# Optimization experiments

Hardware: AMD Instinct MI355X
Metric: run time of the kernel (lower is better)

## Reference

```python
import jax, jax.numpy as jnp
import numpy as np

N = 50000      # nodes
E = 800000     # edges
F_IN = 128     # numInputFeatures
HID = 64       # numHiddenLayerFeatures
C = 40         # numClasses


def setup_inputs() -> dict:
    key = jax.random.key(0)
    ks = jax.random.split(key, 24)
    def nrm(k, shape, s=0.05):
        return jax.random.normal(k, shape, jnp.float32) * s
    return {
        "x": jax.random.normal(ks[0], (N, F_IN), jnp.float32),
        "edge_index": jax.random.randint(ks[1], (2, E), 0, N, jnp.int64),
        "w": jax.random.normal(ks[2], (3,), jnp.float32),  # ensemble weights
        # GCNConv
        "W_gcn": nrm(ks[3], (F_IN, HID)), "b_gcn": jnp.zeros((HID,), jnp.float32),
        # SAGEConv (lin_l on aggregated neighbors w/ bias, lin_r on root no bias)
        "Wl_sage": nrm(ks[4], (F_IN, HID)), "bl_sage": jnp.zeros((HID,), jnp.float32),
        "Wr_sage": nrm(ks[5], (F_IN, HID)),
        # GATConv heads=1
        "W_gat": nrm(ks[6], (F_IN, HID)), "att_src": nrm(ks[7], (HID,)),
        "att_dst": nrm(ks[8], (HID,)), "b_gat": jnp.zeros((HID,), jnp.float32),
        # TransformerConv heads=1 (hidden -> classes)
        "Wq": nrm(ks[9], (HID, C)), "bq": jnp.zeros((C,), jnp.float32),
        "Wk": nrm(ks[10], (HID, C)), "bk": jnp.zeros((C,), jnp.float32),
        "Wv": nrm(ks[11], (HID, C)), "bv": jnp.zeros((C,), jnp.float32),
        "Wskip": nrm(ks[12], (HID, C)), "bskip": jnp.zeros((C,), jnp.float32),
    }


def _segment_softmax(e, seg, num_segments):
    m = jax.ops.segment_max(e, seg, num_segments=num_segments)
    ex = jnp.exp(e - m[seg])
    s = jax.ops.segment_sum(ex, seg, num_segments=num_segments)
    return ex / (s[seg] + 1e-16)


def _gcn(x, src, dst, W, b):
    h = x @ W                                        # [N, HID]
    loop = jnp.arange(N, dtype=src.dtype)
    s = jnp.concatenate([src, loop]); d = jnp.concatenate([dst, loop])
    deg = jax.ops.segment_sum(jnp.ones_like(d, jnp.float32), d, num_segments=N)
    dinv = jnp.where(deg > 0, jax.lax.rsqrt(deg), 0.0)
    norm = dinv[s] * dinv[d]                         # [E+N]
    out = jax.ops.segment_sum(h[s] * norm[:, None], d, num_segments=N)
    return out + b


def _sage(x, src, dst, Wl, bl, Wr):
    cnt = jax.ops.segment_sum(jnp.ones((src.shape[0],), jnp.float32), dst, num_segments=N)
    agg = jax.ops.segment_sum(x[src], dst, num_segments=N) / jnp.maximum(cnt, 1.0)[:, None]
    return agg @ Wl + bl + x @ Wr


def _gat(x, src, dst, W, att_src, att_dst, b):
    h = x @ W                                        # [N, HID]
    loop = jnp.arange(N, dtype=src.dtype)
    s = jnp.concatenate([src, loop]); d = jnp.concatenate([dst, loop])
    a_s = h @ att_src; a_d = h @ att_dst             # [N]
    e = jax.nn.leaky_relu(a_s[s] + a_d[d], 0.2)
    alpha = _segment_softmax(e, d, N)
    out = jax.ops.segment_sum(alpha[:, None] * h[s], d, num_segments=N)
    return out + b


def _transformer(x, src, dst, Wq, bq, Wk, bk, Wv, bv, Wskip, bskip):
    q = x @ Wq + bq; k = x @ Wk + bk; v = x @ Wv + bv  # [N, C]
    score = jnp.sum(q[dst] * k[src], axis=-1) / jnp.sqrt(jnp.float32(C))
    alpha = _segment_softmax(score, dst, N)
    out = jax.ops.segment_sum(alpha[:, None] * v[src], dst, num_segments=N)
    return out + (x @ Wskip + bskip)


def reference(x, edge_index, w, W_gcn, b_gcn, Wl_sage, bl_sage, Wr_sage,
              W_gat, att_src, att_dst, b_gat,
              Wq, bq, Wk, bk, Wv, bv, Wskip, bskip):
    src, dst = edge_index[0], edge_index[1]
    gelu = lambda t: jax.nn.gelu(t, approximate=False)
    ens = gelu(_gcn(x, src, dst, W_gcn, b_gcn)) * w[0]
    ens = ens + gelu(_sage(x, src, dst, Wl_sage, bl_sage, Wr_sage)) * w[1]
    ens = ens + gelu(_gat(x, src, dst, W_gat, att_src, att_dst, b_gat)) * w[2]
    out = _transformer(ens, src, dst, Wq, bq, Wk, bk, Wv, bv, Wskip, bskip)
    return jax.nn.log_softmax(out, axis=1)
```

## Files before the change

### kernel.cpp

```cpp
#include <hip/hip_runtime.h>
#include <math.h>

#define NN 50000
#define EE 800000
#define FIN 128
#define HID 64
#define CL 40
#define SCB 256
#define NBLK ((NN + SCB - 1) / SCB)
#define NREP 8
#define QW 256
#define HGW 192

typedef unsigned short ushort_t;
typedef unsigned int uint_t;
typedef float f32x4 __attribute__((ext_vector_type(4)));
typedef short s16x8 __attribute__((ext_vector_type(8)));

__device__ __forceinline__ ushort_t f2bf(float f) {
  uint_t u = __float_as_uint(f);
  u = (u + 0x7FFFu + ((u >> 16) & 1u)) >> 16;
  return (ushort_t)u;
}
__device__ __forceinline__ uint_t f2bf2(float lo, float hi) {
  return (uint_t)f2bf(lo) | ((uint_t)f2bf(hi) << 16);
}
__device__ __forceinline__ float bf2f(ushort_t s) {
  return __uint_as_float(((uint_t)s) << 16);
}
__device__ __forceinline__ float bflo(uint_t u) {
  return __uint_as_float(u << 16);
}
__device__ __forceinline__ float bfhi(uint_t u) {
  return __uint_as_float(u & 0xFFFF0000u);
}

__device__ __forceinline__ int wave_sum_i(int v) {
#pragma unroll
  for (int off = 32; off > 0; off >>= 1) v += __shfl_xor(v, off, 64);
  return v;
}
__device__ __forceinline__ float half_sum(float v) {
#pragma unroll
  for (int off = 16; off > 0; off >>= 1) v += __shfl_xor(v, off, 64);
  return v;
}
__device__ __forceinline__ float half_max(float v) {
#pragma unroll
  for (int off = 16; off > 0; off >>= 1) v = fmaxf(v, __shfl_xor(v, off, 64));
  return v;
}
__device__ __forceinline__ float gelu_exact(float x) {
  return 0.5f * x * (1.0f + erff(x * 0.70710678118654752f));
}
__device__ __forceinline__ float leaky02(float x) {
  return x >= 0.f ? x : 0.2f * x;
}

#define PREP_W 169
#define PREP_HIST 3125
__global__ __launch_bounds__(256) void k_prep(
    const int* __restrict__ dst,
    const float* __restrict__ W0, const float* __restrict__ W1,
    const float* __restrict__ W2, const float* __restrict__ W3,
    const float* __restrict__ Q0, const float* __restrict__ Q1,
    const float* __restrict__ Q2, const float* __restrict__ Q3,
    const float* __restrict__ b0, const float* __restrict__ b1,
    const float* __restrict__ b2, const float* __restrict__ b3,
    ushort_t* __restrict__ WtA, ushort_t* __restrict__ WtB,
    float* __restrict__ bcat, int* __restrict__ cntR,
    int* __restrict__ erank) {
  int b = blockIdx.x, t = threadIdx.x;
  if (b < PREP_W) {
    int idx = b * 256 + t;
    if (idx < 32768) {
      int m = idx >> 13, r = idx & 8191, c = r >> 7, k = r & 127;
      const float* W = (m == 0) ? W0 : (m == 1) ? W1 : (m == 2) ? W2 : W3;
      WtA[idx] = f2bf(W[k * HID + c]);
    } else if (idx < 43008) {
      int j = idx - 32768;
      int c = j >> 6, k = j & 63;
      int mm = c / CL, cc = c % CL;
      const float* W = (mm == 0) ? Q0 : (mm == 1) ? Q1 : (mm == 2) ? Q2 : Q3;
      WtB[j] = f2bf(W[k * CL + cc]);
    } else if (idx < 43168) {
      int c = idx - 43008;
      int mm = c / CL, cc = c % CL;
      const float* bb = (mm == 0) ? b0 : (mm == 1) ? b1 : (mm == 2) ? b2 : b3;
      bcat[c] = bb[cc];
    }
  } else {
    int hb = b - PREP_W;
    int e = hb * 256 + t;
    if (e < EE) {
      int r = hb & (NREP - 1);
      erank[e] = atomicAdd(&cntR[(size_t)r * NN + dst[e]], 1);
    }
  }
}

__global__ __launch_bounds__(256) void k_gemmA(
    const float* __restrict__ x, const ushort_t* __restrict__ WtA,
    const float* __restrict__ attS, const float* __restrict__ attD,
    ushort_t* __restrict__ Hg, ushort_t* __restrict__ hroot,
    float* __restrict__ a_s, float* __restrict__ a_d) {
  __shared__ __align__(16) ushort_t wlds[64 * 136];
  const int t = threadIdx.x;
  const int wv = t >> 6, l = t & 63;
  const int lr = l & 15, lg = l >> 4;
  const int rbase = blockIdx.x * 64 + wv * 16;
  int arow = rbase + lr;
  int arowc = arow < NN ? arow : NN - 1;
  const float* xp = x + (size_t)arowc * 128 + lg * 8;
  s16x8 af[4];
#pragma unroll
  for (int ks = 0; ks < 4; ++ks) {
    float4 v0 = *(const float4*)(xp + ks * 32);
    float4 v1 = *(const float4*)(xp + ks * 32 + 4);
    s16x8 a;
    a[0] = (short)f2bf(v0.x); a[1] = (short)f2bf(v0.y);
    a[2] = (short)f2bf(v0.z); a[3] = (short)f2bf(v0.w);
    a[4] = (short)f2bf(v1.x); a[5] = (short)f2bf(v1.y);
    a[6] = (short)f2bf(v1.z); a[7] = (short)f2bf(v1.w);
    af[ks] = a;
  }
  for (int m = 0; m < 4; ++m) {
    if (m) __syncthreads();
    for (int idx = t; idx < 64 * 16; idx += 256) {
      int c = idx >> 4, ch = idx & 15;
      *(uint4*)&wlds[c * 136 + ch * 8] =
          *(const uint4*)(WtA + m * 8192 + c * 128 + ch * 8);
    }
    __syncthreads();
    f32x4 acc[4] = {};
#pragma unroll
    for (int ks = 0; ks < 4; ++ks) {
#pragma unroll
      for (int n = 0; n < 4; ++n) {
        s16x8 bf = *(const s16x8*)&wlds[(n * 16 + lr) * 136 + ks * 32 + lg * 8];
        acc[n] =
            __builtin_amdgcn_mfma_f32_16x16x32_bf16(af[ks], bf, acc[n], 0, 0, 0);
      }
    }
#pragma unroll
    for (int n = 0; n < 4; ++n) {
#pragma unroll
      for (int j = 0; j < 4; ++j) {
        int orow = rbase + lg * 4 + j;
        if (orow < NN) {
          if (m < 3)
            Hg[(size_t)orow * HGW + m * 64 + n * 16 + lr] = f2bf(acc[n][j]);
          else
            hroot[(size_t)orow * 64 + n * 16 + lr] = f2bf(acc[n][j]);
        }
      }
    }
    if (m == 2) {
      float sat[4], dat[4];
#pragma unroll
      for (int n = 0; n < 4; ++n) {
        sat[n] = attS[n * 16 + lr];
        dat[n] = attD[n * 16 + lr];
      }
#pragma unroll
      for (int j = 0; j < 4; ++j) {
        float ps = 0.f, pd = 0.f;
#pragma unroll
        for (int n = 0; n < 4; ++n) {
          ps = fmaf(acc[n][j], sat[n], ps);
          pd = fmaf(acc[n][j], dat[n], pd);
        }
#pragma unroll
        for (int off = 1; off < 16; off <<= 1) {
          ps += __shfl_xor(ps, off, 64);
          pd += __shfl_xor(pd, off, 64);
        }
        int orow = rbase + lg * 4 + j;
        if (lr == 0 && orow < NN) { a_s[orow] = ps; a_d[orow] = pd; }
      }
    }
  }
}

__global__ __launch_bounds__(SCB) void k_bsum(const int* __restrict__ cntR,
                                              int* __restrict__ bsum) {
  __shared__ int wsm[4];
  int i = blockIdx.x * SCB + threadIdx.x;
  int v = 0;
  if (i < NN) {
#pragma unroll
    for (int r = 0; r < NREP; ++r) v += cntR[(size_t)r * NN + i];
  }
  int s = wave_sum_i(v);
  int lane = threadIdx.x & 63, wv = threadIdx.x >> 6;
  if (lane == 0) wsm[wv] = s;
  __syncthreads();
  if (threadIdx.x == 0) bsum[blockIdx.x] = wsm[0] + wsm[1] + wsm[2] + wsm[3];
}

__global__ __launch_bounds__(SCB) void k_scanapply(
    const int* __restrict__ cntR, const int* __restrict__ bsum,
    const float* __restrict__ a_s, const float* __restrict__ a_d,
    int* __restrict__ cnt, int* __restrict__ offs, int* __restrict__ base8,
    float* __restrict__ dinv, float2* __restrict__ auxS,
    float2* __restrict__ auxD) {
  __shared__ int ts[SCB];
  __shared__ int wred[4];
  int b = blockIdx.x, t = threadIdx.x;
  int pv = (t < b) ? bsum[t] : 0;
  int ps = wave_sum_i(pv);
  int lane = t & 63, wv = t >> 6;
  if (lane == 0) wred[wv] = ps;
  int i = b * SCB + t;
  int cr[NREP];
  int v = 0;
  if (i < NN) {
#pragma unroll
    for (int r = 0; r < NREP; ++r) {
      cr[r] = cntR[(size_t)r * NN + i];
      v += cr[r];
    }
  }
  ts[t] = v;
  __syncthreads();
  int prefix = wred[0] + wred[1] + wred[2] + wred[3];
  for (int off = 1; off < SCB; off <<= 1) {
    int u = (t >= off) ? ts[t - off] : 0;
    __syncthreads();
    ts[t] += u;
    __syncthreads();
  }
  if (i < NN) {
    int ex = ts[t] - v + prefix;
    offs[i] = ex;
    cnt[i] = v;
    float dv = rsqrtf((float)v + 1.0f);
    dinv[i] = dv;
    auxS[i] = make_float2(dv, a_s[i]);
    auxD[i] = make_float2(dv, a_d[i]);
    int run = ex;
#pragma unroll
    for (int r = 0; r < NREP; ++r) {
      base8[(size_t)i * NREP + r] = run;
      run += cr[r];
    }
  }
}

__global__ __launch_bounds__(256) void k_sc1(const int* __restrict__ dst,
                                             const int* __restrict__ erank,
                                             const int* __restrict__ base8,
                                             int* __restrict__ esorted) {
  int e = blockIdx.x * blockDim.x + threadIdx.x;
  if (e < EE) {
    int d = dst[e];
    int r = (e >> 8) & (NREP - 1);
    esorted[base8[(size_t)d * NREP + r] + erank[e]] = e;
  }
}

__global__ __launch_bounds__(256) void k_sc2(
    const int* __restrict__ esorted, const int* __restrict__ src,
    const int* __restrict__ dst, const float2* __restrict__ auxS,
    const float2* __restrict__ auxD, int* __restrict__ srcidx,
    int* __restrict__ dsts, float2* __restrict__ edata) {
  int p = blockIdx.x * blockDim.x + threadIdx.x;
  if (p < EE) {
    int e = esorted[p];
    int s = src[e], d = dst[e];
    srcidx[p] = s;
    dsts[p] = d;
    float2 A = auxS[s];
    float2 B = auxD[d];
    float ex = __expf(leaky02(A.y + B.y));
    edata[p] = make_float2(A.x * B.x, ex);
  }
}

__global__ __launch_bounds__(256) void k_agg1(
    const int* __restrict__ srcidx, const int* __restrict__ offs,
    const int* __restrict__ cnt, const ushort_t* __restrict__ Hg,
    const ushort_t* __restrict__ hroot, const float2* __restrict__ edata,
    const float* __restrict__ dinv, const float* __restrict__ a_s,
    const float* __restrict__ a_d, const float* __restrict__ b_gcn,
    const float* __restrict__ bl, const float* __restrict__ b_gat,
    const float* __restrict__ w, ushort_t* __restrict__ ensb) {
  int node = (blockIdx.x * blockDim.x + threadIdx.x) >> 6;
  int lane = threadIdx.x & 63;
  if (node >= NN) return;
  const int half = lane >> 5;
  const int fl = lane & 31;
  int beg = offs[node];
  int c = cnt[node];
  int end = beg + c;
  float ag0 = 0.f, ag1 = 0.f, as0 = 0.f, as1 = 0.f, aa0 = 0.f, aa1 = 0.f,
        dg = 0.f;
  int p = beg + half;
  for (; p + 6 < end; p += 8) {
    int sA = srcidx[p], sB = srcidx[p + 2], sC = srcidx[p + 4],
        sD = srcidx[p + 6];
    float2 eA = edata[p], eB = edata[p + 2], eC = edata[p + 4],
           eD = edata[p + 6];
    const uint_t* hA = (const uint_t*)(Hg + (size_t)sA * HGW);
    const uint_t* hB = (const uint_t*)(Hg + (size_t)sB * HGW);
    const uint_t* hC = (const uint_t*)(Hg + (size_t)sC * HGW);
    const uint_t* hD = (const uint_t*)(Hg + (size_t)sD * HGW);
    uint_t gA = hA[fl], qA = hA[32 + fl], tA = hA[64 + fl];
    uint_t gB = hB[fl], qB = hB[32 + fl], tB = hB[64 + fl];
    uint_t gC = hC[fl], qC = hC[32 + fl], tC = hC[64 + fl];
    uint_t gD = hD[fl], qD = hD[32 + fl], tD = hD[64 + fl];
    ag0 = fmaf(bflo(gA), eA.x, ag0); ag1 = fmaf(bfhi(gA), eA.x, ag1);
    ag0 = fmaf(bflo(gB), eB.x, ag0); ag1 = fmaf(bfhi(gB), eB.x, ag1);
    ag0 = fmaf(bflo(gC), eC.x, ag0); ag1 = fmaf(bfhi(gC), eC.x, ag1);
    ag0 = fmaf(bflo(gD), eD.x, ag0); ag1 = fmaf(bfhi(gD), eD.x, ag1);
    as0 += (bflo(qA) + bflo(qB)) + (bflo(qC) + bflo(qD));
    as1 += (bfhi(qA) + bfhi(qB)) + (bfhi(qC) + bfhi(qD));
    aa0 = fmaf(bflo(tA), eA.y, aa0); aa1 = fmaf(bfhi(tA), eA.y, aa1);
    aa0 = fmaf(bflo(tB), eB.y, aa0); aa1 = fmaf(bfhi(tB), eB.y, aa1);
    aa0 = fmaf(bflo(tC), eC.y, aa0); aa1 = fmaf(bfhi(tC), eC.y, aa1);
    aa0 = fmaf(bflo(tD), eD.y, aa0); aa1 = fmaf(bfhi(tD), eD.y, aa1);
    dg += (eA.y + eB.y) + (eC.y + eD.y);
  }
  for (; p < end; p += 2) {
    int sA = srcidx[p];
    float2 eA = edata[p];
    const uint_t* hA = (const uint_t*)(Hg + (size_t)sA * HGW);
    uint_t gA = hA[fl], qA = hA[32 + fl], tA = hA[64 + fl];
    ag0 = fmaf(bflo(gA), eA.x, ag0); ag1 = fmaf(bfhi(gA), eA.x, ag1);
    as0 += bflo(qA);                 as1 += bfhi(qA);
    aa0 = fmaf(bflo(tA), eA.y, aa0); aa1 = fmaf(bfhi(tA), eA.y, aa1);
    dg += eA.y;
  }
  ag0 += __shfl_xor(ag0, 32, 64); ag1 += __shfl_xor(ag1, 32, 64);
  as0 += __shfl_xor(as0, 32, 64); as1 += __shfl_xor(as1, 32, 64);
  aa0 += __shfl_xor(aa0, 32, 64); aa1 += __shfl_xor(aa1, 32, 64);
  dg += __shfl_xor(dg, 32, 64);
  float dd = dinv[node];
  float exl = __expf(leaky02(a_s[node] + a_d[node]));
  const uint_t* hd = (const uint_t*)(Hg + (size_t)node * HGW);
  uint_t hg = hd[fl], ht = hd[64 + fl];
  uint_t hr = ((const uint_t*)hroot)[(size_t)node * 32 + fl];
  float2 bg = ((const float2*)b_gcn)[fl];
  float2 bs = ((const float2*)bl)[fl];
  float2 ba = ((const float2*)b_gat)[fl];
  float dd2 = dd * dd;
  float cinv = 1.0f / fmaxf((float)c, 1.0f);
  float gdi = 1.0f / (dg + exl + 1e-16f);
  float g0 = ag0 + dd2 * bflo(hg) + bg.x;
  float g1 = ag1 + dd2 * bfhi(hg) + bg.y;
  float s0 = as0 * cinv + bs.x + bflo(hr);
  float s1 = as1 * cinv + bs.y + bfhi(hr);
  float t0 = (aa0 + exl * bflo(ht)) * gdi + ba.x;
  float t1 = (aa1 + exl * bfhi(ht)) * gdi + ba.y;
  float w0 = w[0], w1 = w[1], w2 = w[2];
  float e0 = w0 * gelu_exact(g0) + w1 * gelu_exact(s0) + w2 * gelu_exact(t0);
  float e1 = w0 * gelu_exact(g1) + w1 * gelu_exact(s1) + w2 * gelu_exact(t1);
  if (half == 0) ((uint_t*)ensb)[(size_t)node * 32 + fl] = f2bf2(e0, e1);
}

__global__ __launch_bounds__(256) void k_gemmB(
    const ushort_t* __restrict__ ensb, const ushort_t* __restrict__ WtB,
    const float* __restrict__ bcat, ushort_t* __restrict__ QKVSb) {
  __shared__ __align__(16) ushort_t wb[160 * 72];
  __shared__ float bsh[160];
  const int t = threadIdx.x;
  for (int idx = t; idx < 160 * 8; idx += 256) {
    int c = idx >> 3, ch = idx & 7;
    *(uint4*)&wb[c * 72 + ch * 8] = *(const uint4*)(WtB + c * 64 + ch * 8);
  }
  if (t < 160) bsh[t] = bcat[t];
  __syncthreads();
  const int wv = t >> 6, l = t & 63;
  const int lr = l & 15, lg = l >> 4;
  const int rbase = blockIdx.x * 64 + wv * 16;
  int arow = rbase + lr;
  int arowc = arow < NN ? arow : NN - 1;
  const ushort_t* ap = ensb + (size_t)arowc * 64 + lg * 8;
  f32x4 acc[10] = {};
#pragma unroll
  for (int ks = 0; ks < 2; ++ks) {
    s16x8 af = *(const s16x8*)(ap + ks * 32);
#pragma unroll
    for (int n = 0; n < 10; ++n) {
      s16x8 bf = *(const s16x8*)&wb[(n * 16 + lr) * 72 + ks * 32 + lg * 8];
      acc[n] = __builtin_amdgcn_mfma_f32_16x16x32_bf16(af, bf, acc[n], 0, 0, 0);
    }
  }
#pragma unroll
  for (int n = 0; n < 10; ++n) {
    int col = n * 16 + lr;
    int seg = col / CL;
    int off = seg * 64 + (col - seg * CL);
#pragma unroll
    for (int j = 0; j < 4; ++j) {
      int orow = rbase + lg * 4 + j;
      if (orow < NN)
        QKVSb[(size_t)orow * QW + off] = f2bf(acc[n][j] + bsh[col]);
    }
  }
}

__global__ __launch_bounds__(256) void k_score(
    const int* __restrict__ srcidx, const int* __restrict__ dsts,
    const ushort_t* __restrict__ QKVSb, float* __restrict__ escore) {
  int p = (blockIdx.x * 256 + threadIdx.x) >> 3;
  int l = threadIdx.x & 7;
  if (p >= EE) return;
  int s = srcidx[p], d = dsts[p];
  float part = 0.f;
  if (l < 5) {
    const uint4 qv = *(const uint4*)(QKVSb + (size_t)d * QW + l * 8);
    const uint4 kv = *(const uint4*)(QKVSb + (size_t)s * QW + 64 + l * 8);
    part = bflo(qv.x) * bflo(kv.x);
    part = fmaf(bfhi(qv.x), bfhi(kv.x), part);
    part = fmaf(bflo(qv.y), bflo(kv.y), part);
    part = fmaf(bfhi(qv.y), bfhi(kv.y), part);
    part = fmaf(bflo(qv.z), bflo(kv.z), part);
    part = fmaf(bfhi(qv.z), bfhi(kv.z), part);
    part = fmaf(bflo(qv.w), bflo(kv.w), part);
    part = fmaf(bfhi(qv.w), bfhi(kv.w), part);
  }
  part += __shfl_xor(part, 1, 64);
  part += __shfl_xor(part, 2, 64);
  part += __shfl_xor(part, 4, 64);
  if (l == 0) escore[p] = __expf(part * 0.15811388300841897f);
}

__global__ __launch_bounds__(256) void k_agg2(
    const int* __restrict__ srcidx, const int* __restrict__ offs,
    const int* __restrict__ cnt, const ushort_t* __restrict__ QKVSb,
    const float* __restrict__ escore, float* __restrict__ out) {
  int node = (blockIdx.x * blockDim.x + threadIdx.x) >> 6;
  int lane = threadIdx.x & 63;
  if (node >= NN) return;
  const int half = lane >> 5;
  const int fl = lane & 31;
  const bool valid = fl < 20;
  int beg = offs[node];
  int end = beg + cnt[node];
  float den = 0.f, av0 = 0.f, av1 = 0.f;
  const int VOFF = 64;
  int p = beg + half;
  for (; p + 6 < end; p += 8) {
    int sA = srcidx[p], sB = srcidx[p + 2], sC = srcidx[p + 4],
        sD = srcidx[p + 6];
    float eA = escore[p], eB = escore[p + 2], eC = escore[p + 4],
          eD = escore[p + 6];
    uint_t vA = valid ? ((const uint_t*)QKVSb)[(size_t)sA * 128 + VOFF + fl] : 0u;
    uint_t vB = valid ? ((const uint_t*)QKVSb)[(size_t)sB * 128 + VOFF + fl] : 0u;
    uint_t vC = valid ? ((const uint_t*)QKVSb)[(size_t)sC * 128 + VOFF + fl] : 0u;
    uint_t vD = valid ? ((const uint_t*)QKVSb)[(size_t)sD * 128 + VOFF + fl] : 0u;
    av0 = fmaf(eA, bflo(vA), av0); av1 = fmaf(eA, bfhi(vA), av1);
    av0 = fmaf(eB, bflo(vB), av0); av1 = fmaf(eB, bfhi(vB), av1);
    av0 = fmaf(eC, bflo(vC), av0); av1 = fmaf(eC, bfhi(vC), av1);
    av0 = fmaf(eD, bflo(vD), av0); av1 = fmaf(eD, bfhi(vD), av1);
    den += (eA + eB) + (eC + eD);
  }
  for (; p < end; p += 2) {
    int sA = srcidx[p];
    float eA = escore[p];
    uint_t vA = valid ? ((const uint_t*)QKVSb)[(size_t)sA * 128 + VOFF + fl] : 0u;
    av0 = fmaf(eA, bflo(vA), av0); av1 = fmaf(eA, bfhi(vA), av1);
    den += eA;
  }
  av0 += __shfl_xor(av0, 32, 64);
  av1 += __shfl_xor(av1, 32, 64);
  den += __shfl_xor(den, 32, 64);
  uint_t sk = valid ? ((const uint_t*)QKVSb)[(size_t)node * 128 + 96 + fl] : 0u;
  float di = 1.0f / (den + 1e-16f);
  float o0 = valid ? av0 * di + bflo(sk) : -3.0e38f;
  float o1 = valid ? av1 * di + bfhi(sk) : -3.0e38f;
  float m = half_max(fmaxf(o0, o1));
  float eo = valid ? __expf(o0 - m) + __expf(o1 - m) : 0.f;
  float ls = logf(half_sum(eo));
  if (valid && half == 0) {
    float2 r = make_float2(o0 - m - ls, o1 - m - ls);
    ((float2*)out)[(size_t)node * 20 + fl] = r;
  }
}

extern "C" void kernel_launch(void* const* d_in, const int* in_sizes, int n_in,
                              void* d_out, int out_size, void* d_ws,
                              size_t ws_size, hipStream_t stream) {
  const float* x     = (const float*)d_in[0];
  const int*   ei    = (const int*)d_in[1];
  const float* w     = (const float*)d_in[2];
  const float* W_gcn = (const float*)d_in[3];
  const float* b_gcn = (const float*)d_in[4];
  const float* Wl    = (const float*)d_in[5];
  const float* bl    = (const float*)d_in[6];
  const float* Wr    = (const float*)d_in[7];
  const float* W_gat = (const float*)d_in[8];
  const float* att_s = (const float*)d_in[9];
  const float* att_d = (const float*)d_in[10];
  const float* b_gat = (const float*)d_in[11];
  const float* Wq    = (const float*)d_in[12];
  const float* bq    = (const float*)d_in[13];
  const float* Wk    = (const float*)d_in[14];
  const float* bk    = (const float*)d_in[15];
  const float* Wv    = (const float*)d_in[16];
  const float* bv    = (const float*)d_in[17];
  const float* Wsk   = (const float*)d_in[18];
  const float* bsk   = (const float*)d_in[19];
  float* out = (float*)d_out;
  float* ws  = (float*)d_ws;

  const int* src = ei;
  const int* dst = ei + EE;

  ushort_t* Hg     = (ushort_t*)ws;
  ushort_t* hroot  = (ushort_t*)(ws + (size_t)96 * NN);
  ushort_t* ensb   = (ushort_t*)(ws + (size_t)128 * NN);
  float*    a_s    = ws + (size_t)160 * NN;
  float*    a_d    = ws + (size_t)161 * NN;
  float*    dinv   = ws + (size_t)162 * NN;
  ushort_t* qkvsb  = (ushort_t*)(ws + (size_t)163 * NN);
  ushort_t* WtA    = (ushort_t*)(ws + (size_t)291 * NN);
  ushort_t* WtB    = (ushort_t*)(ws + (size_t)291 * NN + 16384);
  float*    bcat   = ws + (size_t)291 * NN + 21504;
  float*    escore = ws + (size_t)291 * NN + 21664;
  float2*   edata  = (float2*)(ws + (size_t)291 * NN + 21664 + EE);
  float2*   auxS   = (float2*)(ws + (size_t)291 * NN + 21664 + 3 * (size_t)EE);
  float2*   auxD   = auxS + NN;
  int*      ibase  = (int*)(ws + (size_t)295 * NN + 21664 + 3 * (size_t)EE);
  int*      cnt    = ibase;
  int*      offs   = ibase + NN;
  int*      srcidx = ibase + 2 * NN;
  int*      dsts   = ibase + 2 * NN + EE;
  int*      erank  = ibase + 2 * NN + 2 * EE;
  int*      esorted= ibase + 2 * NN + 3 * EE;
  int*      bsum   = ibase + 2 * NN + 4 * EE;
  int*      cntR   = ibase + 2 * NN + 4 * EE + 256;
  int*      base8  = cntR + (size_t)NREP * NN;

  hipMemsetAsync(cntR, 0, (size_t)NREP * NN * sizeof(int), stream);

  k_prep<<<PREP_W + PREP_HIST, 256, 0, stream>>>(
      dst, W_gcn, Wl, W_gat, Wr, Wq, Wk, Wv, Wsk, bq, bk, bv, bsk, WtA, WtB,
      bcat, cntR, erank);

  k_gemmA<<<(NN + 63) / 64, 256, 0, stream>>>(x, WtA, att_s, att_d, Hg, hroot,
                                              a_s, a_d);
  k_bsum<<<NBLK, SCB, 0, stream>>>(cntR, bsum);
  k_scanapply<<<NBLK, SCB, 0, stream>>>(cntR, bsum, a_s, a_d, cnt, offs, base8,
                                        dinv, auxS, auxD);
  k_sc1<<<(EE + 255) / 256, 256, 0, stream>>>(dst, erank, base8, esorted);
  k_sc2<<<(EE + 255) / 256, 256, 0, stream>>>(esorted, src, dst, auxS, auxD,
                                              srcidx, dsts, edata);
  k_agg1<<<(NN + 3) / 4, 256, 0, stream>>>(srcidx, offs, cnt, Hg, hroot, edata,
                                           dinv, a_s, a_d, b_gcn, bl, b_gat, w,
                                           ensb);
  k_gemmB<<<(NN + 63) / 64, 256, 0, stream>>>(ensb, WtB, bcat, qkvsb);
  k_score<<<(EE * 8 + 255) / 256, 256, 0, stream>>>(srcidx, dsts, qkvsb,
                                                    escore);
  k_agg2<<<(NN + 3) / 4, 256, 0, stream>>>(srcidx, offs, cnt, qkvsb, escore,
                                           out);
}
```

Before: 219.3 us.

## Aggregate raw bf16 inputs before projecting, and fold attention vectors into weights

```diff
diff --git a/kernel.cpp b/kernel.cpp
--- a/kernel.cpp
+++ b/kernel.cpp
@@ -10,7 +10,6 @@
 #define NBLK ((NN + SCB - 1) / SCB)
 #define NREP 8
 #define QW 256
-#define HGW 192
 
 typedef unsigned short ushort_t;
 typedef unsigned int uint_t;
@@ -25,9 +24,6 @@
 __device__ __forceinline__ uint_t f2bf2(float lo, float hi) {
   return (uint_t)f2bf(lo) | ((uint_t)f2bf(hi) << 16);
 }
-__device__ __forceinline__ float bf2f(ushort_t s) {
-  return __uint_as_float(((uint_t)s) << 16);
-}
 __device__ __forceinline__ float bflo(uint_t u) {
   return __uint_as_float(u << 16);
 }
@@ -36,6 +32,11 @@
 }
 
 __device__ __forceinline__ int wave_sum_i(int v) {
+#pragma unroll
+  for (int off = 32; off > 0; off >>= 1) v += __shfl_xor(v, off, 64);
+  return v;
+}
+__device__ __forceinline__ float wave_sum_f(float v) {
 #pragma unroll
   for (int off = 32; off > 0; off >>= 1) v += __shfl_xor(v, off, 64);
   return v;
@@ -67,9 +68,10 @@
     const float* __restrict__ Q2, const float* __restrict__ Q3,
     const float* __restrict__ b0, const float* __restrict__ b1,
     const float* __restrict__ b2, const float* __restrict__ b3,
+    const float* __restrict__ attS, const float* __restrict__ attD,
     ushort_t* __restrict__ WtA, ushort_t* __restrict__ WtB,
-    float* __restrict__ bcat, int* __restrict__ cntR,
-    int* __restrict__ erank) {
+    float* __restrict__ bcat, float* __restrict__ wv,
+    int* __restrict__ cntR, int* __restrict__ erank) {
   int b = blockIdx.x, t = threadIdx.x;
   if (b < PREP_W) {
     int idx = b * 256 + t;
@@ -89,97 +91,38 @@
       const float* bb = (mm == 0) ? b0 : (mm == 1) ? b1 : (mm == 2) ? b2 : b3;
       bcat[c] = bb[cc];
     }
-  } else {
+  } else if (b < PREP_W + PREP_HIST) {
     int hb = b - PREP_W;
     int e = hb * 256 + t;
     if (e < EE) {
       int r = hb & (NREP - 1);
       erank[e] = atomicAdd(&cntR[(size_t)r * NN + dst[e]], 1);
     }
-  }
-}
-
-__global__ __launch_bounds__(256) void k_gemmA(
-    const float* __restrict__ x, const ushort_t* __restrict__ WtA,
-    const float* __restrict__ attS, const float* __restrict__ attD,
-    ushort_t* __restrict__ Hg, ushort_t* __restrict__ hroot,
-    float* __restrict__ a_s, float* __restrict__ a_d) {
-  __shared__ __align__(16) ushort_t wlds[64 * 136];
-  const int t = threadIdx.x;
-  const int wv = t >> 6, l = t & 63;
-  const int lr = l & 15, lg = l >> 4;
-  const int rbase = blockIdx.x * 64 + wv * 16;
-  int arow = rbase + lr;
-  int arowc = arow < NN ? arow : NN - 1;
-  const float* xp = x + (size_t)arowc * 128 + lg * 8;
-  s16x8 af[4];
-#pragma unroll
-  for (int ks = 0; ks < 4; ++ks) {
-    float4 v0 = *(const float4*)(xp + ks * 32);
-    float4 v1 = *(const float4*)(xp + ks * 32 + 4);
-    s16x8 a;
-    a[0] = (short)f2bf(v0.x); a[1] = (short)f2bf(v0.y);
-    a[2] = (short)f2bf(v0.z); a[3] = (short)f2bf(v0.w);
-    a[4] = (short)f2bf(v1.x); a[5] = (short)f2bf(v1.y);
-    a[6] = (short)f2bf(v1.z); a[7] = (short)f2bf(v1.w);
-    af[ks] = a;
-  }
-  for (int m = 0; m < 4; ++m) {
-    if (m) __syncthreads();
-    for (int idx = t; idx < 64 * 16; idx += 256) {
-      int c = idx >> 4, ch = idx & 15;
-      *(uint4*)&wlds[c * 136 + ch * 8] =
-          *(const uint4*)(WtA + m * 8192 + c * 128 + ch * 8);
-    }
-    __syncthreads();
-    f32x4 acc[4] = {};
-#pragma unroll
-    for (int ks = 0; ks < 4; ++ks) {
-#pragma unroll
-      for (int n = 0; n < 4; ++n) {
-        s16x8 bf = *(const s16x8*)&wlds[(n * 16 + lr) * 136 + ks * 32 + lg * 8];
-        acc[n] =
-            __builtin_amdgcn_mfma_f32_16x16x32_bf16(af[ks], bf, acc[n], 0, 0, 0);
-      }
-    }
-#pragma unroll
-    for (int n = 0; n < 4; ++n) {
-#pragma unroll
-      for (int j = 0; j < 4; ++j) {
-        int orow = rbase + lg * 4 + j;
-        if (orow < NN) {
-          if (m < 3)
-            Hg[(size_t)orow * HGW + m * 64 + n * 16 + lr] = f2bf(acc[n][j]);
-          else
-            hroot[(size_t)orow * 64 + n * 16 + lr] = f2bf(acc[n][j]);
-        }
-      }
-    }
-    if (m == 2) {
-      float sat[4], dat[4];
-#pragma unroll
-      for (int n = 0; n < 4; ++n) {
-        sat[n] = attS[n * 16 + lr];
-        dat[n] = attD[n * 16 + lr];
-      }
-#pragma unroll
-      for (int j = 0; j < 4; ++j) {
-        float ps = 0.f, pd = 0.f;
-#pragma unroll
-        for (int n = 0; n < 4; ++n) {
-          ps = fmaf(acc[n][j], sat[n], ps);
-          pd = fmaf(acc[n][j], dat[n], pd);
-        }
-#pragma unroll
-        for (int off = 1; off < 16; off <<= 1) {
-          ps += __shfl_xor(ps, off, 64);
-          pd += __shfl_xor(pd, off, 64);
-        }
-        int orow = rbase + lg * 4 + j;
-        if (lr == 0 && orow < NN) { a_s[orow] = ps; a_d[orow] = pd; }
-      }
-    }
-  }
+  } else {
+    int which = t >> 7, k = t & 127;
+    const float* att = which ? attD : attS;
+    float s = 0.f;
+    for (int c = 0; c < HID; ++c) s = fmaf(W2[k * HID + c], att[c], s);
+    wv[which * FIN + k] = s;
+  }
+}
+
+__global__ __launch_bounds__(256) void k_xcast(
+    const float* __restrict__ x, const float* __restrict__ wv,
+    uint_t* __restrict__ xbu, float* __restrict__ a_s,
+    float* __restrict__ a_d) {
+  int node = (blockIdx.x * blockDim.x + threadIdx.x) >> 6;
+  int l = threadIdx.x & 63;
+  if (node >= NN) return;
+  float2 xv = ((const float2*)x)[(size_t)node * 64 + l];
+  float2 wsv = ((const float2*)wv)[l];
+  float2 wdv = ((const float2*)(wv + FIN))[l];
+  float ps = fmaf(xv.x, wsv.x, xv.y * wsv.y);
+  float pd = fmaf(xv.x, wdv.x, xv.y * wdv.y);
+  ps = wave_sum_f(ps);
+  pd = wave_sum_f(pd);
+  xbu[(size_t)node * 64 + l] = f2bf2(xv.x, xv.y);
+  if (l == 0) { a_s[node] = ps; a_d[node] = pd; }
 }
 
 __global__ __launch_bounds__(SCB) void k_bsum(const int* __restrict__ cntR,
@@ -277,14 +220,12 @@
   }
 }
 
-__global__ __launch_bounds__(256) void k_agg1(
+__global__ __launch_bounds__(256) void k_agg1x(
     const int* __restrict__ srcidx, const int* __restrict__ offs,
-    const int* __restrict__ cnt, const ushort_t* __restrict__ Hg,
-    const ushort_t* __restrict__ hroot, const float2* __restrict__ edata,
-    const float* __restrict__ dinv, const float* __restrict__ a_s,
-    const float* __restrict__ a_d, const float* __restrict__ b_gcn,
-    const float* __restrict__ bl, const float* __restrict__ b_gat,
-    const float* __restrict__ w, ushort_t* __restrict__ ensb) {
+    const int* __restrict__ cnt, const uint_t* __restrict__ xbu,
+    const float2* __restrict__ edata, const float* __restrict__ dinv,
+    const float* __restrict__ a_s, const float* __restrict__ a_d,
+    uint_t* __restrict__ aggu) {
   int node = (blockIdx.x * blockDim.x + threadIdx.x) >> 6;
   int lane = threadIdx.x & 63;
   if (node >= NN) return;
@@ -293,69 +234,141 @@
   int beg = offs[node];
   int c = cnt[node];
   int end = beg + c;
-  float ag0 = 0.f, ag1 = 0.f, as0 = 0.f, as1 = 0.f, aa0 = 0.f, aa1 = 0.f,
-        dg = 0.f;
+  float g0 = 0.f, g1 = 0.f, g2 = 0.f, g3 = 0.f;
+  float s0 = 0.f, s1 = 0.f, s2 = 0.f, s3 = 0.f;
+  float t0 = 0.f, t1 = 0.f, t2 = 0.f, t3 = 0.f;
+  float dg = 0.f;
   int p = beg + half;
   for (; p + 6 < end; p += 8) {
     int sA = srcidx[p], sB = srcidx[p + 2], sC = srcidx[p + 4],
         sD = srcidx[p + 6];
     float2 eA = edata[p], eB = edata[p + 2], eC = edata[p + 4],
            eD = edata[p + 6];
-    const uint_t* hA = (const uint_t*)(Hg + (size_t)sA * HGW);
-    const uint_t* hB = (const uint_t*)(Hg + (size_t)sB * HGW);
-    const uint_t* hC = (const uint_t*)(Hg + (size_t)sC * HGW);
-    const uint_t* hD = (const uint_t*)(Hg + (size_t)sD * HGW);
-    uint_t gA = hA[fl], qA = hA[32 + fl], tA = hA[64 + fl];
-    uint_t gB = hB[fl], qB = hB[32 + fl], tB = hB[64 + fl];
-    uint_t gC = hC[fl], qC = hC[32 + fl], tC = hC[64 + fl];
-    uint_t gD = hD[fl], qD = hD[32 + fl], tD = hD[64 + fl];
-    ag0 = fmaf(bflo(gA), eA.x, ag0); ag1 = fmaf(bfhi(gA), eA.x, ag1);
-    ag0 = fmaf(bflo(gB), eB.x, ag0); ag1 = fmaf(bfhi(gB), eB.x, ag1);
-    ag0 = fmaf(bflo(gC), eC.x, ag0); ag1 = fmaf(bfhi(gC), eC.x, ag1);
-    ag0 = fmaf(bflo(gD), eD.x, ag0); ag1 = fmaf(bfhi(gD), eD.x, ag1);
-    as0 += (bflo(qA) + bflo(qB)) + (bflo(qC) + bflo(qD));
-    as1 += (bfhi(qA) + bfhi(qB)) + (bfhi(qC) + bfhi(qD));
-    aa0 = fmaf(bflo(tA), eA.y, aa0); aa1 = fmaf(bfhi(tA), eA.y, aa1);
-    aa0 = fmaf(bflo(tB), eB.y, aa0); aa1 = fmaf(bfhi(tB), eB.y, aa1);
-    aa0 = fmaf(bflo(tC), eC.y, aa0); aa1 = fmaf(bfhi(tC), eC.y, aa1);
-    aa0 = fmaf(bflo(tD), eD.y, aa0); aa1 = fmaf(bfhi(tD), eD.y, aa1);
+    const uint_t* xA = xbu + (size_t)sA * 64;
+    const uint_t* xB = xbu + (size_t)sB * 64;
+    const uint_t* xC = xbu + (size_t)sC * 64;
+    const uint_t* xD = xbu + (size_t)sD * 64;
+    uint_t a0 = xA[fl], a1 = xA[32 + fl];
+    uint_t b0 = xB[fl], b1 = xB[32 + fl];
+    uint_t c0 = xC[fl], c1 = xC[32 + fl];
+    uint_t d0 = xD[fl], d1 = xD[32 + fl];
+    float A0 = bflo(a0), A1 = bfhi(a0), A2 = bflo(a1), A3 = bfhi(a1);
+    float B0 = bflo(b0), B1 = bfhi(b0), B2 = bflo(b1), B3 = bfhi(b1);
+    float C0 = bflo(c0), C1 = bfhi(c0), C2 = bflo(c1), C3 = bfhi(c1);
+    float D0 = bflo(d0), D1 = bfhi(d0), D2 = bflo(d1), D3 = bfhi(d1);
+    g0 = fmaf(A0, eA.x, g0); g1 = fmaf(A1, eA.x, g1);
+    g2 = fmaf(A2, eA.x, g2); g3 = fmaf(A3, eA.x, g3);
+    g0 = fmaf(B0, eB.x, g0); g1 = fmaf(B1, eB.x, g1);
+    g2 = fmaf(B2, eB.x, g2); g3 = fmaf(B3, eB.x, g3);
+    g0 = fmaf(C0, eC.x, g0); g1 = fmaf(C1, eC.x, g1);
+    g2 = fmaf(C2, eC.x, g2); g3 = fmaf(C3, eC.x, g3);
+    g0 = fmaf(D0, eD.x, g0); g1 = fmaf(D1, eD.x, g1);
+    g2 = fmaf(D2, eD.x, g2); g3 = fmaf(D3, eD.x, g3);
+    s0 += (A0 + B0) + (C0 + D0); s1 += (A1 + B1) + (C1 + D1);
+    s2 += (A2 + B2) + (C2 + D2); s3 += (A3 + B3) + (C3 + D3);
+    t0 = fmaf(A0, eA.y, t0); t1 = fmaf(A1, eA.y, t1);
+    t2 = fmaf(A2, eA.y, t2); t3 = fmaf(A3, eA.y, t3);
+    t0 = fmaf(B0, eB.y, t0); t1 = fmaf(B1, eB.y, t1);
+    t2 = fmaf(B2, eB.y, t2); t3 = fmaf(B3, eB.y, t3);
+    t0 = fmaf(C0, eC.y, t0); t1 = fmaf(C1, eC.y, t1);
+    t2 = fmaf(C2, eC.y, t2); t3 = fmaf(C3, eC.y, t3);
+    t0 = fmaf(D0, eD.y, t0); t1 = fmaf(D1, eD.y, t1);
+    t2 = fmaf(D2, eD.y, t2); t3 = fmaf(D3, eD.y, t3);
     dg += (eA.y + eB.y) + (eC.y + eD.y);
   }
   for (; p < end; p += 2) {
     int sA = srcidx[p];
     float2 eA = edata[p];
-    const uint_t* hA = (const uint_t*)(Hg + (size_t)sA * HGW);
-    uint_t gA = hA[fl], qA = hA[32 + fl], tA = hA[64 + fl];
-    ag0 = fmaf(bflo(gA), eA.x, ag0); ag1 = fmaf(bfhi(gA), eA.x, ag1);
-    as0 += bflo(qA);                 as1 += bfhi(qA);
-    aa0 = fmaf(bflo(tA), eA.y, aa0); aa1 = fmaf(bfhi(tA), eA.y, aa1);
+    const uint_t* xA = xbu + (size_t)sA * 64;
+    uint_t a0 = xA[fl], a1 = xA[32 + fl];
+    float A0 = bflo(a0), A1 = bfhi(a0), A2 = bflo(a1), A3 = bfhi(a1);
+    g0 = fmaf(A0, eA.x, g0); g1 = fmaf(A1, eA.x, g1);
+    g2 = fmaf(A2, eA.x, g2); g3 = fmaf(A3, eA.x, g3);
+    s0 += A0; s1 += A1; s2 += A2; s3 += A3;
+    t0 = fmaf(A0, eA.y, t0); t1 = fmaf(A1, eA.y, t1);
+    t2 = fmaf(A2, eA.y, t2); t3 = fmaf(A3, eA.y, t3);
     dg += eA.y;
   }
-  ag0 += __shfl_xor(ag0, 32, 64); ag1 += __shfl_xor(ag1, 32, 64);
-  as0 += __shfl_xor(as0, 32, 64); as1 += __shfl_xor(as1, 32, 64);
-  aa0 += __shfl_xor(aa0, 32, 64); aa1 += __shfl_xor(aa1, 32, 64);
+  g0 += __shfl_xor(g0, 32, 64); g1 += __shfl_xor(g1, 32, 64);
+  g2 += __shfl_xor(g2, 32, 64); g3 += __shfl_xor(g3, 32, 64);
+  s0 += __shfl_xor(s0, 32, 64); s1 += __shfl_xor(s1, 32, 64);
+  s2 += __shfl_xor(s2, 32, 64); s3 += __shfl_xor(s3, 32, 64);
+  t0 += __shfl_xor(t0, 32, 64); t1 += __shfl_xor(t1, 32, 64);
+  t2 += __shfl_xor(t2, 32, 64); t3 += __shfl_xor(t3, 32, 64);
   dg += __shfl_xor(dg, 32, 64);
   float dd = dinv[node];
   float exl = __expf(leaky02(a_s[node] + a_d[node]));
-  const uint_t* hd = (const uint_t*)(Hg + (size_t)node * HGW);
-  uint_t hg = hd[fl], ht = hd[64 + fl];
-  uint_t hr = ((const uint_t*)hroot)[(size_t)node * 32 + fl];
-  float2 bg = ((const float2*)b_gcn)[fl];
-  float2 bs = ((const float2*)bl)[fl];
-  float2 ba = ((const float2*)b_gat)[fl];
+  const uint_t* xn = xbu + (size_t)node * 64;
+  uint_t n0 = xn[fl], n1 = xn[32 + fl];
+  float X0 = bflo(n0), X1 = bfhi(n0), X2 = bflo(n1), X3 = bfhi(n1);
   float dd2 = dd * dd;
+  g0 = fmaf(X0, dd2, g0); g1 = fmaf(X1, dd2, g1);
+  g2 = fmaf(X2, dd2, g2); g3 = fmaf(X3, dd2, g3);
+  t0 = fmaf(X0, exl, t0); t1 = fmaf(X1, exl, t1);
+  t2 = fmaf(X2, exl, t2); t3 = fmaf(X3, exl, t3);
   float cinv = 1.0f / fmaxf((float)c, 1.0f);
   float gdi = 1.0f / (dg + exl + 1e-16f);
-  float g0 = ag0 + dd2 * bflo(hg) + bg.x;
-  float g1 = ag1 + dd2 * bfhi(hg) + bg.y;
-  float s0 = as0 * cinv + bs.x + bflo(hr);
-  float s1 = as1 * cinv + bs.y + bfhi(hr);
-  float t0 = (aa0 + exl * bflo(ht)) * gdi + ba.x;
-  float t1 = (aa1 + exl * bfhi(ht)) * gdi + ba.y;
+  s0 *= cinv; s1 *= cinv; s2 *= cinv; s3 *= cinv;
+  t0 *= gdi; t1 *= gdi; t2 *= gdi; t3 *= gdi;
+  if (half == 0) {
+    uint_t* ag = aggu + (size_t)node * 192;
+    ag[fl] = f2bf2(g0, g1);       ag[32 + fl] = f2bf2(g2, g3);
+    ag[64 + fl] = f2bf2(s0, s1);  ag[96 + fl] = f2bf2(s2, s3);
+    ag[128 + fl] = f2bf2(t0, t1); ag[160 + fl] = f2bf2(t2, t3);
+  }
+}
+
+__global__ __launch_bounds__(256) void k_post(
+    const ushort_t* __restrict__ agg, const ushort_t* __restrict__ xb,
+    const ushort_t* __restrict__ WtA, const float* __restrict__ b_gcn,
+    const float* __restrict__ bl, const float* __restrict__ b_gat,
+    const float* __restrict__ w, ushort_t* __restrict__ ensb) {
+  __shared__ __align__(16) ushort_t wlds[64 * 136];
+  const int t = threadIdx.x;
+  const int wv = t >> 6, l = t & 63;
+  const int lr = l & 15, lg = l >> 4;
+  const int rbase = blockIdx.x * 64 + wv * 16;
+  int arow = rbase + lr;
+  int arowc = arow < NN ? arow : NN - 1;
+  f32x4 acc[4][4] = {};
+#pragma unroll
+  for (int m = 0; m < 4; ++m) {
+    if (m) __syncthreads();
+    for (int idx = t; idx < 64 * 16; idx += 256) {
+      int c = idx >> 4, ch = idx & 15;
+      *(uint4*)&wlds[c * 136 + ch * 8] =
+          *(const uint4*)(WtA + m * 8192 + c * 128 + ch * 8);
+    }
+    __syncthreads();
+    const ushort_t* ap = (m < 3) ? agg + (size_t)arowc * 384 + m * 128 + lg * 8
+                                 : xb + (size_t)arowc * 128 + lg * 8;
+#pragma unroll
+    for (int ks = 0; ks < 4; ++ks) {
+      s16x8 af = *(const s16x8*)(ap + ks * 32);
+#pragma unroll
+      for (int n = 0; n < 4; ++n) {
+        s16x8 bf = *(const s16x8*)&wlds[(n * 16 + lr) * 136 + ks * 32 + lg * 8];
+        acc[m][n] =
+            __builtin_amdgcn_mfma_f32_16x16x32_bf16(af, bf, acc[m][n], 0, 0, 0);
+      }
+    }
+  }
   float w0 = w[0], w1 = w[1], w2 = w[2];
-  float e0 = w0 * gelu_exact(g0) + w1 * gelu_exact(s0) + w2 * gelu_exact(t0);
-  float e1 = w0 * gelu_exact(g1) + w1 * gelu_exact(s1) + w2 * gelu_exact(t1);
-  if (half == 0) ((uint_t*)ensb)[(size_t)node * 32 + fl] = f2bf2(e0, e1);
+#pragma unroll
+  for (int n = 0; n < 4; ++n) {
+    int col = n * 16 + lr;
+    float bgv = b_gcn[col], bsv = bl[col], bav = b_gat[col];
+#pragma unroll
+    for (int j = 0; j < 4; ++j) {
+      int orow = rbase + lg * 4 + j;
+      if (orow < NN) {
+        float g = gelu_exact(acc[0][n][j] + bgv);
+        float s = gelu_exact(acc[1][n][j] + acc[3][n][j] + bsv);
+        float tt = gelu_exact(acc[2][n][j] + bav);
+        ensb[(size_t)orow * 64 + col] = f2bf(w0 * g + w1 * s + w2 * tt);
+      }
+    }
+  }
 }
 
 __global__ __launch_bounds__(256) void k_gemmB(
@@ -403,27 +416,25 @@
 __global__ __launch_bounds__(256) void k_score(
     const int* __restrict__ srcidx, const int* __restrict__ dsts,
     const ushort_t* __restrict__ QKVSb, float* __restrict__ escore) {
-  int p = (blockIdx.x * 256 + threadIdx.x) >> 3;
-  int l = threadIdx.x & 7;
+  int p = blockIdx.x * 256 + threadIdx.x;
   if (p >= EE) return;
   int s = srcidx[p], d = dsts[p];
-  float part = 0.f;
-  if (l < 5) {
-    const uint4 qv = *(const uint4*)(QKVSb + (size_t)d * QW + l * 8);
-    const uint4 kv = *(const uint4*)(QKVSb + (size_t)s * QW + 64 + l * 8);
-    part = bflo(qv.x) * bflo(kv.x);
-    part = fmaf(bfhi(qv.x), bfhi(kv.x), part);
-    part = fmaf(bflo(qv.y), bflo(kv.y), part);
-    part = fmaf(bfhi(qv.y), bfhi(kv.y), part);
-    part = fmaf(bflo(qv.z), bflo(kv.z), part);
-    part = fmaf(bfhi(qv.z), bfhi(kv.z), part);
-    part = fmaf(bflo(qv.w), bflo(kv.w), part);
-    part = fmaf(bfhi(qv.w), bfhi(kv.w), part);
-  }
-  part += __shfl_xor(part, 1, 64);
-  part += __shfl_xor(part, 2, 64);
-  part += __shfl_xor(part, 4, 64);
-  if (l == 0) escore[p] = __expf(part * 0.15811388300841897f);
+  const uint4* qp = (const uint4*)(QKVSb + (size_t)d * QW);
+  const uint4* kp = (const uint4*)(QKVSb + (size_t)s * QW + 64);
+  float dot = 0.f;
+#pragma unroll
+  for (int i = 0; i < 5; ++i) {
+    uint4 q = qp[i], k = kp[i];
+    dot = fmaf(bflo(q.x), bflo(k.x), dot);
+    dot = fmaf(bfhi(q.x), bfhi(k.x), dot);
+    dot = fmaf(bflo(q.y), bflo(k.y), dot);
+    dot = fmaf(bfhi(q.y), bfhi(k.y), dot);
+    dot = fmaf(bflo(q.z), bflo(k.z), dot);
+    dot = fmaf(bfhi(q.z), bfhi(k.z), dot);
+    dot = fmaf(bflo(q.w), bflo(k.w), dot);
+    dot = fmaf(bfhi(q.w), bfhi(k.w), dot);
+  }
+  escore[p] = __expf(dot * 0.15811388300841897f);
 }
 
 __global__ __launch_bounds__(256) void k_agg2(
@@ -508,21 +519,22 @@
   const int* src = ei;
   const int* dst = ei + EE;
 
-  ushort_t* Hg     = (ushort_t*)ws;
-  ushort_t* hroot  = (ushort_t*)(ws + (size_t)96 * NN);
-  ushort_t* ensb   = (ushort_t*)(ws + (size_t)128 * NN);
-  float*    a_s    = ws + (size_t)160 * NN;
-  float*    a_d    = ws + (size_t)161 * NN;
-  float*    dinv   = ws + (size_t)162 * NN;
-  ushort_t* qkvsb  = (ushort_t*)(ws + (size_t)163 * NN);
-  ushort_t* WtA    = (ushort_t*)(ws + (size_t)291 * NN);
-  ushort_t* WtB    = (ushort_t*)(ws + (size_t)291 * NN + 16384);
-  float*    bcat   = ws + (size_t)291 * NN + 21504;
-  float*    escore = ws + (size_t)291 * NN + 21664;
-  float2*   edata  = (float2*)(ws + (size_t)291 * NN + 21664 + EE);
-  float2*   auxS   = (float2*)(ws + (size_t)291 * NN + 21664 + 3 * (size_t)EE);
-  float2*   auxD   = auxS + NN;
-  int*      ibase  = (int*)(ws + (size_t)295 * NN + 21664 + 3 * (size_t)EE);
+  uint_t*   xbu    = (uint_t*)ws;
+  uint_t*   aggu   = (uint_t*)(ws + (size_t)64 * NN);
+  ushort_t* ensb   = (ushort_t*)(ws + (size_t)256 * NN);
+  float*    a_s    = ws + (size_t)288 * NN;
+  float*    a_d    = ws + (size_t)289 * NN;
+  float*    dinv   = ws + (size_t)290 * NN;
+  ushort_t* qkvsb  = (ushort_t*)(ws + (size_t)291 * NN);
+  float2*   auxS   = (float2*)(ws + (size_t)419 * NN);
+  float2*   auxD   = (float2*)(ws + (size_t)421 * NN);
+  float*    wv     = ws + (size_t)423 * NN;
+  ushort_t* WtA    = (ushort_t*)(ws + (size_t)423 * NN + 256);
+  ushort_t* WtB    = (ushort_t*)(ws + (size_t)423 * NN + 16640);
+  float*    bcat   = ws + (size_t)423 * NN + 21760;
+  float*    escore = ws + (size_t)423 * NN + 21920;
+  float2*   edata  = (float2*)(ws + (size_t)423 * NN + 21920 + EE);
+  int*      ibase  = (int*)(ws + (size_t)423 * NN + 21920 + 3 * (size_t)EE);
   int*      cnt    = ibase;
   int*      offs   = ibase + NN;
   int*      srcidx = ibase + 2 * NN;
@@ -535,24 +547,24 @@
 
   hipMemsetAsync(cntR, 0, (size_t)NREP * NN * sizeof(int), stream);
 
-  k_prep<<<PREP_W + PREP_HIST, 256, 0, stream>>>(
-      dst, W_gcn, Wl, W_gat, Wr, Wq, Wk, Wv, Wsk, bq, bk, bv, bsk, WtA, WtB,
-      bcat, cntR, erank);
-
-  k_gemmA<<<(NN + 63) / 64, 256, 0, stream>>>(x, WtA, att_s, att_d, Hg, hroot,
-                                              a_s, a_d);
+  k_prep<<<PREP_W + PREP_HIST + 1, 256, 0, stream>>>(
+      dst, W_gcn, Wl, W_gat, Wr, Wq, Wk, Wv, Wsk, bq, bk, bv, bsk, att_s,
+      att_d, WtA, WtB, bcat, wv, cntR, erank);
+
+  k_xcast<<<(NN + 3) / 4, 256, 0, stream>>>(x, wv, xbu, a_s, a_d);
   k_bsum<<<NBLK, SCB, 0, stream>>>(cntR, bsum);
   k_scanapply<<<NBLK, SCB, 0, stream>>>(cntR, bsum, a_s, a_d, cnt, offs, base8,
                                         dinv, auxS, auxD);
   k_sc1<<<(EE + 255) / 256, 256, 0, stream>>>(dst, erank, base8, esorted);
   k_sc2<<<(EE + 255) / 256, 256, 0, stream>>>(esorted, src, dst, auxS, auxD,
                                               srcidx, dsts, edata);
-  k_agg1<<<(NN + 3) / 4, 256, 0, stream>>>(srcidx, offs, cnt, Hg, hroot, edata,
-                                           dinv, a_s, a_d, b_gcn, bl, b_gat, w,
-                                           ensb);
+  k_agg1x<<<(NN + 3) / 4, 256, 0, stream>>>(srcidx, offs, cnt, xbu, edata,
+                                            dinv, a_s, a_d, aggu);
+  k_post<<<(NN + 63) / 64, 256, 0, stream>>>((const ushort_t*)aggu,
+                                             (const ushort_t*)xbu, WtA, b_gcn,
+                                             bl, b_gat, w, ensb);
   k_gemmB<<<(NN + 63) / 64, 256, 0, stream>>>(ensb, WtB, bcat, qkvsb);
-  k_score<<<(EE * 8 + 255) / 256, 256, 0, stream>>>(srcidx, dsts, qkvsb,
-                                                    escore);
+  k_score<<<(EE + 255) / 256, 256, 0, stream>>>(srcidx, dsts, qkvsb, escore);
   k_agg2<<<(NN + 3) / 4, 256, 0, stream>>>(srcidx, offs, cnt, qkvsb, escore,
                                            out);
 }
```

After: 225.4 us. 1.03x slower.
